# Kernel optimization log

Measured on AMD Instinct MI355X. Metric: run time of the kernel, lower is better.

The kernel has to match this reference:

```python
import math
import jax, jax.numpy as jnp
import numpy as np

B, L, D, H = 8, 2048, 512, 8  # batch, seq_len, d_model, num_heads
DEPTH = D // H


def setup_inputs() -> dict:
    key = jax.random.key(0)
    ks = jax.random.split(key, 7)
    s = 1.0 / np.sqrt(D)
    return {
        "q": jax.random.normal(ks[0], (B, L, D), jnp.float32),
        "k": jax.random.normal(ks[1], (B, L, D), jnp.float32),
        "v": jax.random.normal(ks[2], (B, L, D), jnp.float32),
        "Wq": jax.random.normal(ks[3], (D, D), jnp.float32) * s,
        "bq": jnp.zeros((D,), jnp.float32),
        "Wk": jax.random.normal(ks[4], (D, D), jnp.float32) * s,
        "bk": jnp.zeros((D,), jnp.float32),
        "Wv": jax.random.normal(ks[5], (D, D), jnp.float32) * s,
        "bv": jnp.zeros((D,), jnp.float32),
        "Wo": jax.random.normal(ks[6], (D, D), jnp.float32) * s,
        "bo": jnp.zeros((D,), jnp.float32),
    }


def reference(q, k, v, Wq, bq, Wk, bk, Wv, bv, Wo, bo):
    b, l, d = q.shape

    def split_heads(x, W, bias):
        y = x @ W + bias                      # [B,L,D]
        return jnp.transpose(y.reshape(b, l, H, DEPTH), (0, 2, 1, 3))  # [B,H,L,depth]

    qh = split_heads(q, Wq, bq)
    kh = split_heads(k, Wk, bk)
    vh = split_heads(v, Wv, bv)  # computed (as in original) but unused in aggregation
    del vh

    # L == S here so the pad/truncate branch is a no-op.
    qt = jnp.transpose(qh, (0, 1, 3, 2))      # [B,H,depth,L]
    kt = jnp.transpose(kh, (0, 1, 3, 2))

    # Period-based correlation via FFT: R_qk = irfft(rfft(q) * conj(rfft(k)))
    R_qk = jnp.fft.irfft(jnp.fft.rfft(qt) * jnp.conj(jnp.fft.rfft(kt)), n=l)

    top_k = int(2 * math.log(l))              # = 15 for L=2048
    weights, indices = jax.lax.top_k(R_qk, top_k)   # [B,H,depth,top_k]
    corr = jax.nn.softmax(weights, axis=-1)

    t = jnp.arange(l)
    delays_agg = jnp.zeros_like(qt)
    for i in range(top_k):  # small fixed loop over top-k delays
        pos = (t[None, None, None, :] + indices[..., i:i + 1]) % l  # circular gather index
        pattern = jnp.take_along_axis(qt, pos, axis=-1)
        delays_agg = delays_agg + pattern * corr[..., i:i + 1]

    out = jnp.transpose(delays_agg, (0, 3, 1, 2)).reshape(b, l, d)  # [B,L,D]
    return out @ Wo + bo
```

## Files before the change

kernel.cpp:

```cpp
#include <hip/hip_runtime.h>
#include <hip/hip_fp16.h>
#include <float.h>
#include <math.h>

#define BB 8
#define LL 2048
#define NN 2048
#define MM 1024
#define DD 512
#define HH 8
#define DEPTH 64
#define TOPK 15
#define PIF 3.14159265358979323846f

#define PD(i) ((i) + ((i) >> 5))

using f16x8 = __attribute__((ext_vector_type(8))) _Float16;
typedef __attribute__((ext_vector_type(4))) float f32x4;
typedef __attribute__((ext_vector_type(8))) unsigned short us8;
typedef __attribute__((ext_vector_type(4))) unsigned short us4;

__device__ __forceinline__ unsigned short f2h(float f) {
    return __half_as_ushort(__float2half(f));
}
__device__ __forceinline__ float h2f(unsigned short u) {
    return (float)__builtin_bit_cast(_Float16, u);
}
__device__ __forceinline__ float2 cmul(float2 a, float2 b) {
    return make_float2(a.x * b.x - a.y * b.y, a.x * b.y + a.y * b.x);
}
__device__ __forceinline__ float2 cmulc(float2 a, float2 b) {
    return make_float2(a.x * b.x + a.y * b.y, a.y * b.x - a.x * b.y);
}
__device__ __forceinline__ float2 cadd(float2 a, float2 b) { return make_float2(a.x + b.x, a.y + b.y); }
__device__ __forceinline__ float2 csub(float2 a, float2 b) { return make_float2(a.x - b.x, a.y - b.y); }

__device__ __forceinline__ void xcd_swizzle_512(int bx, int by, int& obx, int& oby) {
    int flat = by * 4 + bx;
    int xcd = flat & 7;
    int pos = flat >> 3;
    int nid = xcd * 64 + pos;
    obx = nid & 3;
    oby = nid >> 2;
}

__global__ __launch_bounds__(256) void wt_convert(const float* __restrict__ Wq,
                                                  const float* __restrict__ Wk,
                                                  const float* __restrict__ Wo,
                                                  unsigned short* __restrict__ Tq,
                                                  unsigned short* __restrict__ Tk,
                                                  unsigned short* __restrict__ To) {
    __shared__ float T[64][65];
    const float* src = blockIdx.z == 0 ? Wq : (blockIdx.z == 1 ? Wk : Wo);
    unsigned short* dst = blockIdx.z == 0 ? Tq : (blockIdx.z == 1 ? Tk : To);
    const int tid = threadIdx.x;
    const int r0 = blockIdx.y * 64, c0 = blockIdx.x * 64;
#pragma unroll
    for (int p = 0; p < 4; ++p) {
        int idx = tid + 256 * p;
        int row = idx >> 4, c4 = idx & 15;
        float4 v = *reinterpret_cast<const float4*>(&src[(size_t)(r0 + row) * DD + c0 + c4 * 4]);
        T[row][c4 * 4 + 0] = v.x;
        T[row][c4 * 4 + 1] = v.y;
        T[row][c4 * 4 + 2] = v.z;
        T[row][c4 * 4 + 3] = v.w;
    }
    __syncthreads();
#pragma unroll
    for (int p = 0; p < 4; ++p) {
        int idx = tid + 256 * p;
        int orow = idx >> 4, oc4 = idx & 15;
        us4 o;
#pragma unroll
        for (int j = 0; j < 4; ++j) o[j] = f2h(T[oc4 * 4 + j][orow]);
        *reinterpret_cast<us4*>(&dst[(size_t)(c0 + orow) * DD + r0 + oc4 * 4]) = o;
    }
}

__global__ __launch_bounds__(256) void proj_gemm_mfma(const float* __restrict__ X,
                                                      const unsigned short* __restrict__ Wt,
                                                      const float* __restrict__ bias,
                                                      unsigned short* __restrict__ outT) {
    __shared__ unsigned short Asm[128][40];
    __shared__ unsigned short Bsm[128][40];
    const int tid = threadIdx.x;
    const int lane = tid & 63, wid = tid >> 6;
    const int wM = wid & 1, wN = wid >> 1;
    const int g = lane >> 4, rl = lane & 15;
    int sbx, sby;
    xcd_swizzle_512(blockIdx.x, blockIdx.y, sbx, sby);
    const int r0 = sby * 128, c0 = sbx * 128;
    f32x4 acc[4][4];
#pragma unroll
    for (int m = 0; m < 4; ++m)
#pragma unroll
        for (int n = 0; n < 4; ++n) acc[m][n] = (f32x4){0.f, 0.f, 0.f, 0.f};

    for (int k0 = 0; k0 < DD; k0 += 32) {
        float4 av[4];
#pragma unroll
        for (int p = 0; p < 4; ++p) {
            int idx = tid + 256 * p;
            int row = idx >> 3, kq = idx & 7;
            av[p] = *reinterpret_cast<const float4*>(&X[(size_t)(r0 + row) * DD + k0 + kq * 4]);
        }
        us8 bv[2];
#pragma unroll
        for (int p = 0; p < 2; ++p) {
            int idx = tid + 256 * p;
            int row = idx >> 2, kq = idx & 3;
            bv[p] = *reinterpret_cast<const us8*>(&Wt[(size_t)(c0 + row) * DD + k0 + kq * 8]);
        }
        __syncthreads();
#pragma unroll
        for (int p = 0; p < 4; ++p) {
            int idx = tid + 256 * p;
            int row = idx >> 3, kq = idx & 7;
            us4 w;
            w[0] = f2h(av[p].x); w[1] = f2h(av[p].y); w[2] = f2h(av[p].z); w[3] = f2h(av[p].w);
            *reinterpret_cast<us4*>(&Asm[row][kq * 4]) = w;
        }
#pragma unroll
        for (int p = 0; p < 2; ++p) {
            int idx = tid + 256 * p;
            int row = idx >> 2, kq = idx & 3;
            *reinterpret_cast<us8*>(&Bsm[row][kq * 8]) = bv[p];
        }
        __syncthreads();
        f16x8 af[4], bfr[4];
#pragma unroll
        for (int m = 0; m < 4; ++m)
            af[m] = *reinterpret_cast<const f16x8*>(&Bsm[wM * 64 + m * 16 + rl][g * 8]);
#pragma unroll
        for (int n = 0; n < 4; ++n)
            bfr[n] = *reinterpret_cast<const f16x8*>(&Asm[wN * 64 + n * 16 + rl][g * 8]);
#pragma unroll
        for (int m = 0; m < 4; ++m)
#pragma unroll
            for (int n = 0; n < 4; ++n)
                acc[m][n] = __builtin_amdgcn_mfma_f32_16x16x32_f16(af[m], bfr[n], acc[m][n], 0, 0, 0);
    }

    const int b = r0 >> 11, l0 = r0 & (LL - 1);
#pragma unroll
    for (int m = 0; m < 4; ++m) {
        int cb = c0 + wM * 64 + m * 16 + g * 4;
        float4 bv4 = *reinterpret_cast<const float4*>(&bias[cb]);
        const float bja[4] = {bv4.x, bv4.y, bv4.z, bv4.w};
#pragma unroll
        for (int j = 0; j < 4; ++j) {
            int c = cb + j;
            int h = c >> 6, dd = c & 63;
            unsigned short* orow = &outT[((size_t)(b * HH + h) * DEPTH + dd) * LL];
#pragma unroll
            for (int n = 0; n < 4; ++n) {
                int l = l0 + wN * 64 + n * 16 + rl;
                orow[l] = f2h(acc[m][n][j] + bja[j]);
            }
        }
    }
}

__global__ __launch_bounds__(256) void corr_fft_v7(const unsigned short* __restrict__ qt,
                                                   unsigned short* __restrict__ kt) {
    __shared__ float zr[2112], zi[2112];
    __shared__ float twr[1056], twi[1056];
    __shared__ float sLB[4];
    __shared__ int cnt;
    __shared__ float corr_s[TOPK];
    __shared__ int topi_s[TOPK];
    const int tid = threadIdx.x;
    const int lane = tid & 63, wid = tid >> 6;
    const size_t base = (size_t)blockIdx.x * NN;

#define LD2(i) make_float2(zr[i], zi[i])
#define ST2(i, v) do { zr[i] = (v).x; zi[i] = (v).y; } while (0)

    {
        us8 qa = *reinterpret_cast<const us8*>(qt + base + 8 * tid);
        us8 ka = *reinterpret_cast<const us8*>(kt + base + 8 * tid);
        f16x8 qh = __builtin_bit_cast(f16x8, qa);
        f16x8 kh = __builtin_bit_cast(f16x8, ka);
        int pb = (int)(__brev((unsigned)tid) >> 24);
        const int b3[8] = {0, 4, 2, 6, 1, 5, 3, 7};
#pragma unroll
        for (int u = 0; u < 8; ++u) {
            int pf = b3[u] * 256 + pb;
            zr[PD(pf)] = (float)qh[u];
            zi[PD(pf)] = (float)kh[u];
        }
#pragma unroll
        for (int v = 0; v < 4; ++v) {
            int j = tid + 256 * v;
            float sn, cs;
            __sincosf(-PIF * (float)j * (1.f / 1024.f), &sn, &cs);
            twr[PD(j)] = cs;
            twi[PD(j)] = sn;
        }
    }
    __syncthreads();

#pragma unroll
    for (int i2 = 0; i2 < 2; ++i2) {
        int q = tid + 256 * i2;
        int i0 = q << 2;
        int e0 = PD(i0), e1 = PD(i0 + 1), e2 = PD(i0 + 2), e3 = PD(i0 + 3);
        float2 a = LD2(e0), b = LD2(e1), c = LD2(e2), d = LD2(e3);
        float2 A0 = cadd(a, b), A1 = csub(a, b), A2 = cadd(c, d), A3 = csub(c, d);
        float2 t3 = make_float2(A3.y, -A3.x);
        ST2(e0, cadd(A0, A2));
        ST2(e2, csub(A0, A2));
        ST2(e1, cadd(A1, t3));
        ST2(e3, csub(A1, t3));
    }
    __syncthreads();
#pragma unroll
    for (int hh = 4; hh <= 64; hh <<= 2) {
        const int step = 512 / hh;
#pragma unroll
        for (int i2 = 0; i2 < 2; ++i2) {
            int q = tid + 256 * i2;
            int p = q & (hh - 1);
            int i0 = ((q ^ p) << 2) | p;
            int e0 = PD(i0), e1 = PD(i0 + hh), e2 = PD(i0 + 2 * hh), e3 = PD(i0 + 3 * hh);
            float2 a = LD2(e0), b = LD2(e1), c = LD2(e2), d = LD2(e3);
            int jt = PD(p * step);
            float2 w2 = make_float2(twr[jt], twi[jt]);
            float2 w1 = make_float2(w2.x * w2.x - w2.y * w2.y, 2.f * w2.x * w2.y);
            float2 bp = cmul(b, w1), dp = cmul(d, w1);
            float2 A0 = cadd(a, bp), A1 = csub(a, bp);
            float2 A2 = cadd(c, dp), A3 = csub(c, dp);
            float2 t2 = cmul(A2, w2);
            float2 u3 = cmul(A3, w2);
            float2 t3 = make_float2(u3.y, -u3.x);
            ST2(e0, cadd(A0, t2));
            ST2(e2, csub(A0, t2));
            ST2(e1, cadd(A1, t3));
            ST2(e3, csub(A1, t3));
        }
        __syncthreads();
    }
    {
        float2 z[8];
#pragma unroll
        for (int u = 0; u < 8; ++u) z[u] = LD2(PD(tid + 256 * u));
        {
            int j = PD(4 * tid);
            float2 wa = make_float2(twr[j], twi[j]);
#pragma unroll
            for (int a2 = 0; a2 < 4; ++a2) {
                float2 tv = cmul(z[2 * a2 + 1], wa);
                z[2 * a2 + 1] = csub(z[2 * a2], tv);
                z[2 * a2] = cadd(z[2 * a2], tv);
            }
        }
        {
            int j = PD(2 * tid);
            float2 wb = make_float2(twr[j], twi[j]);
            float2 wbn = make_float2(wb.y, -wb.x);
#pragma unroll
            for (int kk = 0; kk < 4; ++kk) {
                const int u0a[4] = {0, 1, 4, 5};
                int u0 = u0a[kk];
                float2 w = (kk & 1) ? wbn : wb;
                float2 tv = cmul(z[u0 + 2], w);
                z[u0 + 2] = csub(z[u0], tv);
                z[u0] = cadd(z[u0], tv);
            }
        }
        {
            int j = PD(tid);
            float2 wc = make_float2(twr[j], twi[j]);
            const float R2 = 0.70710678118654752f;
            float2 wt0 = wc;
            float2 wt1 = cmul(wc, make_float2(R2, -R2));
            float2 wt2 = make_float2(wc.y, -wc.x);
            float2 wt3 = cmul(wc, make_float2(-R2, -R2));
            float2 tv;
            tv = cmul(z[4], wt0); z[4] = csub(z[0], tv); z[0] = cadd(z[0], tv);
            tv = cmul(z[5], wt1); z[5] = csub(z[1], tv); z[1] = cadd(z[1], tv);
            tv = cmul(z[6], wt2); z[6] = csub(z[2], tv); z[2] = cadd(z[2], tv);
            tv = cmul(z[7], wt3); z[7] = csub(z[3], tv); z[3] = cadd(z[3], tv);
        }
#pragma unroll
        for (int u = 0; u < 8; ++u) ST2(PD(tid + 256 * u), z[u]);
    }
    __syncthreads();

    {
        float2 W[4];
#pragma unroll
        for (int u = 0; u < 4; ++u) {
            int m = tid + 256 * u;
            int mf1 = (NN - m) & (NN - 1);
            float2 Zf = LD2(PD(m)), Zm = LD2(PD(mf1));
            float2 Qf = make_float2(0.5f * (Zf.x + Zm.x), 0.5f * (Zf.y - Zm.y));
            float2 Dm = make_float2(Zf.x - Zm.x, Zf.y + Zm.y);
            float2 Kf = make_float2(0.5f * Dm.y, -0.5f * Dm.x);
            float2 S1 = cmulc(Qf, Kf);
            float2 Zf2 = LD2(PD(m + MM)), Zm2 = LD2(PD(MM - m));
            float2 Qf2 = make_float2(0.5f * (Zf2.x + Zm2.x), 0.5f * (Zf2.y - Zm2.y));
            float2 Dm2 = make_float2(Zf2.x - Zm2.x, Zf2.y + Zm2.y);
            float2 Kf2 = make_float2(0.5f * Dm2.y, -0.5f * Dm2.x);
            float2 S2 = cmulc(Qf2, Kf2);
            float2 E = cadd(S1, S2), Od = csub(S1, S2);
            int jm = PD(m);
            float2 ph = make_float2(twr[jm], -twi[jm]);
            float2 T = cmul(ph, Od);
            W[u] = make_float2(E.x - T.y, E.y + T.x);
        }
        int j = PD(2 * tid);
        float2 w = make_float2(twr[j], -twi[j]);
        float2 w2 = make_float2(w.x * w.x - w.y * w.y, 2.f * w.x * w.y);
        float2 S0 = cadd(W[0], W[2]);
        float2 D0 = cmul(csub(W[0], W[2]), w);
        float2 S1q = cadd(W[1], W[3]);
        float2 ff = cmul(csub(W[1], W[3]), w);
        float2 D1 = make_float2(-ff.y, ff.x);
        float2 o0 = cadd(S0, S1q);
        float2 o1 = cmul(csub(S0, S1q), w2);
        float2 o2 = cadd(D0, D1);
        float2 o3 = cmul(csub(D0, D1), w2);
        __syncthreads();
        ST2(PD(tid), o0);
        ST2(PD(tid + 256), o1);
        ST2(PD(tid + 512), o2);
        ST2(PD(tid + 768), o3);
    }
    __syncthreads();

#pragma unroll
    for (int hh = 64; hh >= 4; hh >>= 2) {
        const int step = 512 / hh;
        int q = tid;
        int p = q & (hh - 1);
        int i0 = ((q ^ p) << 2) | p;
        int e0 = PD(i0), e1 = PD(i0 + hh), e2 = PD(i0 + 2 * hh), e3 = PD(i0 + 3 * hh);
        float2 a = LD2(e0), b = LD2(e1), c = LD2(e2), d = LD2(e3);
        int jt = PD(p * step);
        float2 w = make_float2(twr[jt], -twi[jt]);
        float2 w2 = make_float2(w.x * w.x - w.y * w.y, 2.f * w.x * w.y);
        float2 S0 = cadd(a, c);
        float2 D0 = cmul(csub(a, c), w);
        float2 S1 = cadd(b, d);
        float2 ff = cmul(csub(b, d), w);
        float2 D1 = make_float2(-ff.y, ff.x);
        ST2(e0, cadd(S0, S1));
        ST2(e1, cmul(csub(S0, S1), w2));
        ST2(e2, cadd(D0, D1));
        ST2(e3, cmul(csub(D0, D1), w2));
        __syncthreads();
    }
    float r[8];
    int tau[8];
    {
        float2 a = LD2(PD(4 * tid)), b = LD2(PD(4 * tid + 1));
        float2 c = LD2(PD(4 * tid + 2)), d = LD2(PD(4 * tid + 3));
        float2 S0 = cadd(a, c), D0 = csub(a, c);
        float2 S1 = cadd(b, d);
        float2 bd = csub(b, d);
        float2 D1 = make_float2(-bd.y, bd.x);
        float2 z0 = cadd(S0, S1);
        float2 z1 = csub(S0, S1);
        float2 z2 = cadd(D0, D1);
        float2 z3 = csub(D0, D1);
        const int pb = (int)(__brev((unsigned)tid) >> 24);
        const float sc = 1.0f / (float)NN;
        int m0 = pb;
        int m1 = 512 + pb;
        int m2 = 256 + pb;
        int m3 = 768 + pb;
        r[0] = z0.x * sc; tau[0] = 2 * m0;
        r[1] = z0.y * sc; tau[1] = 2 * m0 + 1;
        r[2] = z1.x * sc; tau[2] = 2 * m1;
        r[3] = z1.y * sc; tau[3] = 2 * m1 + 1;
        r[4] = z2.x * sc; tau[4] = 2 * m2;
        r[5] = z2.y * sc; tau[5] = 2 * m2 + 1;
        r[6] = z3.x * sc; tau[6] = 2 * m3;
        r[7] = z3.y * sc; tau[7] = 2 * m3 + 1;
    }

    {
        float lmax = r[0];
#pragma unroll
        for (int u = 1; u < 8; ++u) lmax = fmaxf(lmax, r[u]);
        float sv = lmax;
#pragma unroll
        for (int k = 2; k <= 64; k <<= 1) {
#pragma unroll
            for (int j = k >> 1; j > 0; j >>= 1) {
                float ov = __shfl_xor(sv, j);
                bool lower = (lane & j) == 0;
                bool dirAsc = (lane & k) == 0;
                bool myMinKey = sv > ov;
                bool keepMine = (dirAsc == lower) ? myMinKey : !myMinKey;
                sv = keepMine ? sv : ov;
            }
        }
        float LBw = __shfl(sv, 14);
        if (lane == 0) sLB[wid] = LBw;
        if (tid == 0) cnt = 0;
    }
    __syncthreads();
    {
        float LB = fmaxf(fmaxf(sLB[0], sLB[1]), fmaxf(sLB[2], sLB[3]));
#pragma unroll
        for (int u = 0; u < 8; ++u) {
            if (r[u] >= LB) {
                int slot = atomicAdd(&cnt, 1);
                zr[slot] = r[u];
                zi[slot] = __int_as_float(tau[u]);
            }
        }
    }
    __syncthreads();
    const int ncand = cnt;
    if (tid < 64) {
        float cv;
        int ci;
        if (ncand <= 64) {
            cv = (lane < ncand) ? zr[lane] : -FLT_MAX;
            ci = (lane < ncand) ? __float_as_int(zi[lane]) : 0x7fffffff;
#pragma unroll
            for (int k = 2; k <= 64; k <<= 1) {
#pragma unroll
                for (int j = k >> 1; j > 0; j >>= 1) {
                    float ov = __shfl_xor(cv, j);
                    int oi = __shfl_xor(ci, j);
                    bool lower = (lane & j) == 0;
                    bool dirAsc = (lane & k) == 0;
                    bool myMinKey = (cv > ov) || (cv == ov && ci < oi);
                    bool keepMine = (dirAsc == lower) ? myMinKey : !myMinKey;
                    cv = keepMine ? cv : ov;
                    ci = keepMine ? ci : oi;
                }
            }
        } else {
            float keep_v = -FLT_MAX;
            int keep_i = 0x7fffffff;
            for (int it = 0; it < TOPK; ++it) {
                float bv = -FLT_MAX;
                int bi = 0x7fffffff, bs = 0;
                for (int s = lane; s < ncand; s += 64) {
                    float v = zr[s];
                    int ii = __float_as_int(zi[s]);
                    if (v > bv || (v == bv && ii < bi)) { bv = v; bi = ii; bs = s; }
                }
#pragma unroll
                for (int off = 32; off >= 1; off >>= 1) {
                    float ov = __shfl_xor(bv, off);
                    int oi = __shfl_xor(bi, off);
                    int os = __shfl_xor(bs, off);
                    if (ov > bv || (ov == bv && oi < bi)) { bv = ov; bi = oi; bs = os; }
                }
                if ((bs & 63) == lane) zr[bs] = -FLT_MAX;
                if (lane == it) { keep_v = bv; keep_i = bi; }
            }
            cv = keep_v;
            ci = keep_i;
        }
        float m0 = __shfl(cv, 0);
        float e = (lane < TOPK) ? expf(cv - m0) : 0.f;
        float ssum = e;
#pragma unroll
        for (int off = 32; off >= 1; off >>= 1) ssum += __shfl_xor(ssum, off);
        if (lane < TOPK) {
            corr_s[lane] = e / ssum;
            topi_s[lane] = ci;
        }
    }
    __syncthreads();

    {
        float cw[TOPK];
        int ci[TOPK];
#pragma unroll
        for (int i = 0; i < TOPK; ++i) { cw[i] = corr_s[i]; ci[i] = topi_s[i]; }
        const unsigned short* qrow = qt + base;
#pragma unroll
        for (int u = 0; u < 8; ++u) {
            int t = tid + 256 * u;
            float acc = 0.f;
#pragma unroll
            for (int i = 0; i < TOPK; ++i)
                acc += cw[i] * h2f(qrow[(t + ci[i]) & (NN - 1)]);
            kt[base + t] = f2h(acc);
        }
    }
#undef LD2
#undef ST2
}

__global__ __launch_bounds__(256) void out_gemm_mfma(const unsigned short* __restrict__ db,
                                                     const unsigned short* __restrict__ WtO,
                                                     const float* __restrict__ bias,
                                                     float* __restrict__ out) {
    __shared__ unsigned short Asm[32][132];
    __shared__ unsigned short Bsm[128][40];
    const int tid = threadIdx.x;
    const int lane = tid & 63, wid = tid >> 6;
    const int wr = wid >> 1, wc = wid & 1;
    const int g = lane >> 4, rl = lane & 15;
    int sbx, sby;
    xcd_swizzle_512(blockIdx.x, blockIdx.y, sbx, sby);
    const int r0 = sby * 128, c0 = sbx * 128;
    const int b = r0 >> 11, l0 = r0 & (LL - 1);
    f32x4 acc[4][4];
#pragma unroll
    for (int m = 0; m < 4; ++m)
#pragma unroll
        for (int n = 0; n < 4; ++n) acc[m][n] = (f32x4){0.f, 0.f, 0.f, 0.f};

    for (int k0 = 0; k0 < DD; k0 += 32) {
        us8 avv[2], bvv[2];
#pragma unroll
        for (int p = 0; p < 2; ++p) {
            int idx = tid + 256 * p;
            int kr = idx >> 4, dc = idx & 15;
            avv[p] = *reinterpret_cast<const us8*>(
                &db[(size_t)(b * DD + k0 + kr) * 2048 + l0 + dc * 8]);
        }
#pragma unroll
        for (int p = 0; p < 2; ++p) {
            int idx = tid + 256 * p;
            int row = idx >> 2, kq = idx & 3;
            bvv[p] = *reinterpret_cast<const us8*>(&WtO[(size_t)(c0 + row) * DD + k0 + kq * 8]);
        }
        __syncthreads();
#pragma unroll
        for (int p = 0; p < 2; ++p) {
            int idx = tid + 256 * p;
            int kr = idx >> 4, dc = idx & 15;
            us4 lo, hi;
#pragma unroll
            for (int j = 0; j < 4; ++j) { lo[j] = avv[p][j]; hi[j] = avv[p][j + 4]; }
            *reinterpret_cast<us4*>(&Asm[kr][dc * 8]) = lo;
            *reinterpret_cast<us4*>(&Asm[kr][dc * 8 + 4]) = hi;
        }
#pragma unroll
        for (int p = 0; p < 2; ++p) {
            int idx = tid + 256 * p;
            int row = idx >> 2, kq = idx & 3;
            *reinterpret_cast<us8*>(&Bsm[row][kq * 8]) = bvv[p];
        }
        __syncthreads();
        f16x8 af[4], bfr[4];
#pragma unroll
        for (int m = 0; m < 4; ++m) {
            int l = wr * 64 + m * 16 + rl;
            us8 t;
#pragma unroll
            for (int j = 0; j < 8; ++j) t[j] = Asm[g * 8 + j][l];
            af[m] = __builtin_bit_cast(f16x8, t);
        }
#pragma unroll
        for (int n = 0; n < 4; ++n)
            bfr[n] = *reinterpret_cast<const f16x8*>(&Bsm[wc * 64 + n * 16 + rl][g * 8]);
#pragma unroll
        for (int m = 0; m < 4; ++m)
#pragma unroll
            for (int n = 0; n < 4; ++n)
                acc[m][n] = __builtin_amdgcn_mfma_f32_16x16x32_f16(af[m], bfr[n], acc[m][n], 0, 0, 0);
    }

#pragma unroll
    for (int m = 0; m < 4; ++m) {
#pragma unroll
        for (int n = 0; n < 4; ++n) {
            int c = c0 + wc * 64 + n * 16 + rl;
            float bvv = bias[c];
            int rbase = r0 + wr * 64 + m * 16 + g * 4;
#pragma unroll
            for (int j = 0; j < 4; ++j)
                out[(size_t)(rbase + j) * DD + c] = acc[m][n][j] + bvv;
        }
    }
}

extern "C" void kernel_launch(void* const* d_in, const int* in_sizes, int n_in,
                              void* d_out, int out_size, void* d_ws, size_t ws_size,
                              hipStream_t stream) {
    const float* q = (const float*)d_in[0];
    const float* k = (const float*)d_in[1];
    const float* Wq = (const float*)d_in[3];
    const float* bq = (const float*)d_in[4];
    const float* Wk = (const float*)d_in[5];
    const float* bk = (const float*)d_in[6];
    const float* Wo = (const float*)d_in[9];
    const float* bo = (const float*)d_in[10];
    float* out = (float*)d_out;

    unsigned short* qt = (unsigned short*)d_ws;
    unsigned short* kt = qt + (size_t)BB * HH * DEPTH * LL;
    unsigned short* Tq = kt + (size_t)BB * HH * DEPTH * LL;
    unsigned short* Tk = Tq + (size_t)DD * DD;
    unsigned short* To = Tk + (size_t)DD * DD;

    dim3 blk(256);
    wt_convert<<<dim3(8, 8, 3), blk, 0, stream>>>(Wq, Wk, Wo, Tq, Tk, To);
    proj_gemm_mfma<<<dim3(4, 128), blk, 0, stream>>>(q, Tq, bq, qt);
    proj_gemm_mfma<<<dim3(4, 128), blk, 0, stream>>>(k, Tk, bk, kt);
    corr_fft_v7<<<dim3(BB * HH * DEPTH), blk, 0, stream>>>(qt, kt);
    out_gemm_mfma<<<dim3(4, 128), blk, 0, stream>>>(kt, To, bo, out);
}
```

Before: 144.4 us.

## Merge projection GEMMs, use radix-8 FFT stages, vectorize delay aggregation

Fuses the two Q/K projection GEMM launches into one launch using blockIdx.z, cutting a launch and improving occupancy. The forward FFT's radix-4 passes are regrouped into radix-8 passes, which reduces the number of shared-memory passes and barriers. The delay aggregation now loads two aligned 8-wide vectors per delay and selects elements via a switch, then writes 8 outputs in one store. The out-GEMM shared tile is also padded differently to change bank mapping. These changes add code complexity and switch divergence in exchange.

```diff
diff --git a/kernel.cpp b/kernel.cpp
--- a/kernel.cpp
+++ b/kernel.cpp
@@ -77,10 +77,19 @@
     }
 }
 
-__global__ __launch_bounds__(256) void proj_gemm_mfma(const float* __restrict__ X,
-                                                      const unsigned short* __restrict__ Wt,
-                                                      const float* __restrict__ bias,
-                                                      unsigned short* __restrict__ outT) {
+__global__ __launch_bounds__(256) void proj_gemm2(const float* __restrict__ Xq,
+                                                  const float* __restrict__ Xk,
+                                                  const unsigned short* __restrict__ Tq,
+                                                  const unsigned short* __restrict__ Tk,
+                                                  const float* __restrict__ bq,
+                                                  const float* __restrict__ bk,
+                                                  unsigned short* __restrict__ qt,
+                                                  unsigned short* __restrict__ kt) {
+    const float* X = blockIdx.z == 0 ? Xq : Xk;
+    const unsigned short* Wt = blockIdx.z == 0 ? Tq : Tk;
+    const float* bias = blockIdx.z == 0 ? bq : bk;
+    unsigned short* outT = blockIdx.z == 0 ? qt : kt;
+
     __shared__ unsigned short Asm[128][40];
     __shared__ unsigned short Bsm[128][40];
     const int tid = threadIdx.x;
@@ -161,7 +170,7 @@
     }
 }
 
-__global__ __launch_bounds__(256) void corr_fft_v7(const unsigned short* __restrict__ qt,
+__global__ __launch_bounds__(256) void corr_fft_v8(const unsigned short* __restrict__ qt,
                                                    unsigned short* __restrict__ kt) {
     __shared__ float zr[2112], zi[2112];
     __shared__ float twr[1056], twi[1056];
@@ -172,6 +181,7 @@
     const int tid = threadIdx.x;
     const int lane = tid & 63, wid = tid >> 6;
     const size_t base = (size_t)blockIdx.x * NN;
+    const float R2 = 0.70710678118654752f;
 
 #define LD2(i) make_float2(zr[i], zi[i])
 #define ST2(i, v) do { zr[i] = (v).x; zi[i] = (v).y; } while (0)
@@ -200,67 +210,64 @@
     }
     __syncthreads();
 
-#pragma unroll
-    for (int i2 = 0; i2 < 2; ++i2) {
-        int q = tid + 256 * i2;
-        int i0 = q << 2;
-        int e0 = PD(i0), e1 = PD(i0 + 1), e2 = PD(i0 + 2), e3 = PD(i0 + 3);
-        float2 a = LD2(e0), b = LD2(e1), c = LD2(e2), d = LD2(e3);
-        float2 A0 = cadd(a, b), A1 = csub(a, b), A2 = cadd(c, d), A3 = csub(c, d);
-        float2 t3 = make_float2(A3.y, -A3.x);
-        ST2(e0, cadd(A0, A2));
-        ST2(e2, csub(A0, A2));
-        ST2(e1, cadd(A1, t3));
-        ST2(e3, csub(A1, t3));
-    }
-    __syncthreads();
-#pragma unroll
-    for (int hh = 4; hh <= 64; hh <<= 2) {
-        const int step = 512 / hh;
-#pragma unroll
-        for (int i2 = 0; i2 < 2; ++i2) {
-            int q = tid + 256 * i2;
-            int p = q & (hh - 1);
-            int i0 = ((q ^ p) << 2) | p;
-            int e0 = PD(i0), e1 = PD(i0 + hh), e2 = PD(i0 + 2 * hh), e3 = PD(i0 + 3 * hh);
-            float2 a = LD2(e0), b = LD2(e1), c = LD2(e2), d = LD2(e3);
-            int jt = PD(p * step);
-            float2 w2 = make_float2(twr[jt], twi[jt]);
-            float2 w1 = make_float2(w2.x * w2.x - w2.y * w2.y, 2.f * w2.x * w2.y);
-            float2 bp = cmul(b, w1), dp = cmul(d, w1);
-            float2 A0 = cadd(a, bp), A1 = csub(a, bp);
-            float2 A2 = cadd(c, dp), A3 = csub(c, dp);
-            float2 t2 = cmul(A2, w2);
-            float2 u3 = cmul(A3, w2);
-            float2 t3 = make_float2(u3.y, -u3.x);
-            ST2(e0, cadd(A0, t2));
-            ST2(e2, csub(A0, t2));
-            ST2(e1, cadd(A1, t3));
-            ST2(e3, csub(A1, t3));
-        }
-        __syncthreads();
-    }
-    {
+    {
+        int i0 = tid << 3;
         float2 z[8];
 #pragma unroll
-        for (int u = 0; u < 8; ++u) z[u] = LD2(PD(tid + 256 * u));
+        for (int u = 0; u < 8; ++u) z[u] = LD2(PD(i0 + u));
+#pragma unroll
+        for (int a = 0; a < 4; ++a) {
+            float2 tv = z[2 * a + 1];
+            z[2 * a + 1] = csub(z[2 * a], tv);
+            z[2 * a] = cadd(z[2 * a], tv);
+        }
         {
-            int j = PD(4 * tid);
-            float2 wa = make_float2(twr[j], twi[j]);
-#pragma unroll
-            for (int a2 = 0; a2 < 4; ++a2) {
-                float2 tv = cmul(z[2 * a2 + 1], wa);
-                z[2 * a2 + 1] = csub(z[2 * a2], tv);
-                z[2 * a2] = cadd(z[2 * a2], tv);
+            const int u0a[4] = {0, 1, 4, 5};
+#pragma unroll
+            for (int kk = 0; kk < 4; ++kk) {
+                int u0 = u0a[kk];
+                float2 s = z[u0 + 2];
+                float2 tv = (kk & 1) ? make_float2(s.y, -s.x) : s;
+                z[u0 + 2] = csub(z[u0], tv);
+                z[u0] = cadd(z[u0], tv);
             }
         }
         {
-            int j = PD(2 * tid);
-            float2 wb = make_float2(twr[j], twi[j]);
+            float2 tv;
+            tv = z[4];                                              z[4] = csub(z[0], tv); z[0] = cadd(z[0], tv);
+            tv = cmul(z[5], make_float2(R2, -R2));                  z[5] = csub(z[1], tv); z[1] = cadd(z[1], tv);
+            { float2 s = z[6]; tv = make_float2(s.y, -s.x); }       z[6] = csub(z[2], tv); z[2] = cadd(z[2], tv);
+            tv = cmul(z[7], make_float2(-R2, -R2));                 z[7] = csub(z[3], tv); z[3] = cadd(z[3], tv);
+        }
+#pragma unroll
+        for (int u = 0; u < 8; ++u) ST2(PD(i0 + u), z[u]);
+    }
+    __syncthreads();
+
+#pragma unroll
+    for (int hh = 8; hh <= 64; hh <<= 3) {
+        int p = tid & (hh - 1);
+        int i0 = ((tid ^ p) << 3) | p;
+        float2 z[8];
+#pragma unroll
+        for (int u = 0; u < 8; ++u) z[u] = LD2(PD(i0 + hh * u));
+        int ja = PD(p * (1024 / hh));
+        float2 wa = make_float2(twr[ja], twi[ja]);
+        int jb = PD(p * (512 / hh));
+        float2 wb = make_float2(twr[jb], twi[jb]);
+        int jc = PD(p * (256 / hh));
+        float2 wc = make_float2(twr[jc], twi[jc]);
+#pragma unroll
+        for (int a = 0; a < 4; ++a) {
+            float2 tv = cmul(z[2 * a + 1], wa);
+            z[2 * a + 1] = csub(z[2 * a], tv);
+            z[2 * a] = cadd(z[2 * a], tv);
+        }
+        {
             float2 wbn = make_float2(wb.y, -wb.x);
+            const int u0a[4] = {0, 1, 4, 5};
 #pragma unroll
             for (int kk = 0; kk < 4; ++kk) {
-                const int u0a[4] = {0, 1, 4, 5};
                 int u0 = u0a[kk];
                 float2 w = (kk & 1) ? wbn : wb;
                 float2 tv = cmul(z[u0 + 2], w);
@@ -269,9 +276,42 @@
             }
         }
         {
+            float2 wt0 = wc;
+            float2 wt1 = cmul(wc, make_float2(R2, -R2));
+            float2 wt2 = make_float2(wc.y, -wc.x);
+            float2 wt3 = cmul(wc, make_float2(-R2, -R2));
+            float2 tv;
+            tv = cmul(z[4], wt0); z[4] = csub(z[0], tv); z[0] = cadd(z[0], tv);
+            tv = cmul(z[5], wt1); z[5] = csub(z[1], tv); z[1] = cadd(z[1], tv);
+            tv = cmul(z[6], wt2); z[6] = csub(z[2], tv); z[2] = cadd(z[2], tv);
+            tv = cmul(z[7], wt3); z[7] = csub(z[3], tv); z[3] = cadd(z[3], tv);
+        }
+#pragma unroll
+        for (int u = 0; u < 8; ++u) ST2(PD(i0 + hh * u), z[u]);
+        __syncthreads();
+    }
+
+    {
+        float2 z[8];
+#pragma unroll
+        for (int u = 0; u < 8; ++u) z[u] = LD2(PD(tid + 256 * u));
+        {
+            int j = PD(2 * tid);
+            float2 wb = make_float2(twr[j], twi[j]);
+            float2 wbn = make_float2(wb.y, -wb.x);
+            const int u0a[4] = {0, 1, 4, 5};
+#pragma unroll
+            for (int kk = 0; kk < 4; ++kk) {
+                int u0 = u0a[kk];
+                float2 w = (kk & 1) ? wbn : wb;
+                float2 tv = cmul(z[u0 + 2], w);
+                z[u0 + 2] = csub(z[u0], tv);
+                z[u0] = cadd(z[u0], tv);
+            }
+        }
+        {
             int j = PD(tid);
             float2 wc = make_float2(twr[j], twi[j]);
-            const float R2 = 0.70710678118654752f;
             float2 wt0 = wc;
             float2 wt1 = cmul(wc, make_float2(R2, -R2));
             float2 wt2 = make_float2(wc.y, -wc.x);
@@ -332,9 +372,8 @@
 #pragma unroll
     for (int hh = 64; hh >= 4; hh >>= 2) {
         const int step = 512 / hh;
-        int q = tid;
-        int p = q & (hh - 1);
-        int i0 = ((q ^ p) << 2) | p;
+        int p = tid & (hh - 1);
+        int i0 = ((tid ^ p) << 2) | p;
         int e0 = PD(i0), e1 = PD(i0 + hh), e2 = PD(i0 + 2 * hh), e3 = PD(i0 + 3 * hh);
         float2 a = LD2(e0), b = LD2(e1), c = LD2(e2), d = LD2(e3);
         int jt = PD(p * step);
@@ -366,10 +405,7 @@
         float2 z3 = csub(D0, D1);
         const int pb = (int)(__brev((unsigned)tid) >> 24);
         const float sc = 1.0f / (float)NN;
-        int m0 = pb;
-        int m1 = 512 + pb;
-        int m2 = 256 + pb;
-        int m3 = 768 + pb;
+        int m0 = pb, m1 = 512 + pb, m2 = 256 + pb, m3 = 768 + pb;
         r[0] = z0.x * sc; tau[0] = 2 * m0;
         r[1] = z0.y * sc; tau[1] = 2 * m0 + 1;
         r[2] = z1.x * sc; tau[2] = 2 * m1;
@@ -472,20 +508,34 @@
     __syncthreads();
 
     {
-        float cw[TOPK];
-        int ci[TOPK];
-#pragma unroll
-        for (int i = 0; i < TOPK; ++i) { cw[i] = corr_s[i]; ci[i] = topi_s[i]; }
         const unsigned short* qrow = qt + base;
-#pragma unroll
-        for (int u = 0; u < 8; ++u) {
-            int t = tid + 256 * u;
-            float acc = 0.f;
-#pragma unroll
-            for (int i = 0; i < TOPK; ++i)
-                acc += cw[i] * h2f(qrow[(t + ci[i]) & (NN - 1)]);
-            kt[base + t] = f2h(acc);
-        }
+        const int t0 = tid << 3;
+        float acc8[8] = {0.f, 0.f, 0.f, 0.f, 0.f, 0.f, 0.f, 0.f};
+        for (int i = 0; i < TOPK; ++i) {
+            const float w = corr_s[i];
+            const int d = topi_s[i];
+            const int s = (t0 + d) & (NN - 1);
+            const int a0 = s & ~7;
+            const int o = s & 7;
+            us8 A = *reinterpret_cast<const us8*>(qrow + a0);
+            us8 Bv = *reinterpret_cast<const us8*>(qrow + ((a0 + 8) & (NN - 1)));
+            switch (o) {
+#define AGG_CASE(O)                                                              \
+    case O: {                                                                    \
+        _Pragma("unroll") for (int j = 0; j < 8; ++j) {                          \
+            unsigned short e = ((O) + j < 8) ? A[(O) + j] : Bv[(O) + j - 8];     \
+            acc8[j] += w * h2f(e);                                               \
+        }                                                                        \
+    } break;
+                AGG_CASE(0) AGG_CASE(1) AGG_CASE(2) AGG_CASE(3)
+                AGG_CASE(4) AGG_CASE(5) AGG_CASE(6) AGG_CASE(7)
+#undef AGG_CASE
+            }
+        }
+        us8 o8;
+#pragma unroll
+        for (int j = 0; j < 8; ++j) o8[j] = f2h(acc8[j]);
+        *reinterpret_cast<us8*>(kt + base + t0) = o8;
     }
 #undef LD2
 #undef ST2
@@ -495,7 +545,7 @@
                                                      const unsigned short* __restrict__ WtO,
                                                      const float* __restrict__ bias,
                                                      float* __restrict__ out) {
-    __shared__ unsigned short Asm[32][132];
+    __shared__ unsigned short Asm[32][134];
     __shared__ unsigned short Bsm[128][40];
     const int tid = threadIdx.x;
     const int lane = tid & 63, wid = tid >> 6;
@@ -598,8 +648,7 @@
 
     dim3 blk(256);
     wt_convert<<<dim3(8, 8, 3), blk, 0, stream>>>(Wq, Wk, Wo, Tq, Tk, To);
-    proj_gemm_mfma<<<dim3(4, 128), blk, 0, stream>>>(q, Tq, bq, qt);
-    proj_gemm_mfma<<<dim3(4, 128), blk, 0, stream>>>(k, Tk, bk, kt);
-    corr_fft_v7<<<dim3(BB * HH * DEPTH), blk, 0, stream>>>(qt, kt);
+    proj_gemm2<<<dim3(4, 128, 2), blk, 0, stream>>>(q, k, Tq, Tk, bq, bk, qt, kt);
+    corr_fft_v8<<<dim3(BB * HH * DEPTH), blk, 0, stream>>>(qt, kt);
     out_gemm_mfma<<<dim3(4, 128), blk, 0, stream>>>(kt, To, bo, out);
 }
```

Result: faster. 125.8 us (-12.8%).
